# Optimization experiments

Hardware: AMD Instinct MI355X
Metric: run time of the kernel (lower is better)

The kernel has to match this reference:

```python
import jax, jax.numpy as jnp
import numpy as np
import math

B, H, W, C = 8, 32, 32, 512
NUM_HEAD_CHANNELS = 64
NUM_HEADS = C // NUM_HEAD_CHANNELS  # 8
HEAD_DIM = C // NUM_HEADS            # 64
NUM_GROUPS = max(1, C // 16)         # 32
EPS = 1e-6  # flax GroupNorm default epsilon


def setup_inputs() -> dict:
    key = jax.random.key(0)
    ks = jax.random.split(key, 7)
    s = lambda fan: 1.0 / math.sqrt(fan)
    return {
        "x": jax.random.normal(ks[0], (B, H, W, C), jnp.float32),
        "gn_scale": jnp.ones((C,), jnp.float32),
        "gn_bias": jnp.zeros((C,), jnp.float32),
        "w_qkv": jax.random.normal(ks[1], (C, 3 * C), jnp.float32) * s(C),
        "b_qkv": jnp.zeros((3 * C,), jnp.float32),
        "w_out": jax.random.normal(ks[2], (C, C), jnp.float32) * s(C),
        "b_out": jnp.zeros((C,), jnp.float32),
    }


def _group_norm(x, scale, bias):
    # x: (B,H,W,C); normalize per (batch, group) over spatial + in-group channels
    b, h, w, c = x.shape
    xg = x.reshape(b, h * w, NUM_GROUPS, c // NUM_GROUPS)
    mu = jnp.mean(xg, axis=(1, 3), keepdims=True)
    var = jnp.var(xg, axis=(1, 3), keepdims=True)
    xn = (xg - mu) * jax.lax.rsqrt(var + EPS)
    return xn.reshape(b, h, w, c) * scale + bias


def reference(x, gn_scale, gn_bias, w_qkv, b_qkv, w_out, b_out):
    b, h, w, c = x.shape
    seq = h * w
    x_flat = x.reshape(b, seq, c)
    x_norm = _group_norm(x, gn_scale, gn_bias).reshape(b, seq, c)
    qkv = x_norm @ w_qkv + b_qkv                      # (b, seq, 3c)
    q, k, v = jnp.split(qkv, 3, axis=-1)
    scale = 1.0 / math.sqrt(HEAD_DIM)

    def to_heads(t):
        return t.reshape(b, seq, NUM_HEADS, HEAD_DIM).transpose(0, 2, 1, 3)

    q, k, v = to_heads(q), to_heads(k), to_heads(v)
    # NOTE: scale applied to both q and k, matching the original module
    weight = jnp.einsum('bhld,bhsd->bhls', q * scale, k * scale)
    weight = jax.nn.softmax(weight, axis=-1)
    out = jnp.einsum('bhls,bhsd->bhld', weight, v)
    out = out.transpose(0, 2, 1, 3).reshape(b, seq, c)
    out = out @ w_out + b_out
    return (x_flat + out).reshape(b, h, w, c)
```

## Files before the change

kernel.cpp:

```cpp
#include <hip/hip_runtime.h>
#include <hip/hip_bf16.h>

#define SEQ   1024
#define CH    512
#define NHEAD 8
#define HDIM  64
#define BATCH 8

using short8  = __attribute__((ext_vector_type(8))) short;
using short4v = __attribute__((ext_vector_type(4))) short;
using floatx4 = __attribute__((ext_vector_type(4))) float;

__device__ inline unsigned short f2bf(float f) {
  __hip_bfloat16 h = __float2bfloat16(f);
  return __builtin_bit_cast(unsigned short, h);
}

__device__ inline void load_lds16(const void* g, void* l) {
  __builtin_amdgcn_global_load_lds(
      (const __attribute__((address_space(1))) unsigned int*)g,
      (__attribute__((address_space(3))) unsigned int*)l, 16, 0, 0);
}

__global__ __launch_bounds__(256) void prep_kernel(
    const float* __restrict__ wqkv, const float* __restrict__ wout,
    const float* __restrict__ x, const float* __restrict__ gsc,
    const float* __restrict__ gbs,
    unsigned short* __restrict__ wqkvt, unsigned short* __restrict__ woutt,
    unsigned short* __restrict__ xn) {
  __shared__ float SH[32 * 33 + 8];
  const int blk = blockIdx.x, tid = threadIdx.x;

  if (blk >= 256) {
    const float* src; unsigned short* dst; int C, bx, by;
    if (blk < 1024) { int t = blk - 256; src = wqkv; dst = wqkvt; C = 1536; bx = t % 48; by = t / 48; }
    else { int t = blk - 1024; src = wout; dst = woutt; C = 512; bx = t & 15; by = t >> 4; }
    float (*T)[33] = (float(*)[33])SH;
    int tx = tid & 31, ty = tid >> 5;
    for (int j = 0; j < 4; ++j)
      T[ty + j * 8][tx] = src[(size_t)(by * 32 + ty + j * 8) * C + bx * 32 + tx];
    __syncthreads();
    for (int j = 0; j < 4; ++j)
      dst[(size_t)(bx * 32 + ty + j * 8) * 512 + by * 32 + tx] = f2bf(T[tx][ty + j * 8]);
    return;
  }

  int bg = blk;
  int b = bg >> 5, g = bg & 31;
  const size_t base = (size_t)b * SEQ * CH + g * 16;

  float4 v[16];
  float s = 0.f, sq = 0.f;
  for (int i = 0; i < 16; ++i) {
    int c = i * 256 + tid;
    int r = c >> 2, c4 = (c & 3) * 4;
    v[i] = *(const float4*)(x + base + (size_t)r * CH + c4);
    s  += v[i].x + v[i].y + v[i].z + v[i].w;
    sq += v[i].x * v[i].x + v[i].y * v[i].y + v[i].z * v[i].z + v[i].w * v[i].w;
  }
  for (int off = 1; off < 64; off <<= 1) {
    s  += __shfl_xor(s, off);
    sq += __shfl_xor(sq, off);
  }
  float* ls = SH + 1056;
  float* lq = SH + 1060;
  int wid = tid >> 6, lane = tid & 63;
  if (lane == 0) { ls[wid] = s; lq[wid] = sq; }
  __syncthreads();
  float ts = ls[0] + ls[1] + ls[2] + ls[3];
  float tq = lq[0] + lq[1] + lq[2] + lq[3];
  const float inv_n = 1.0f / 16384.0f;
  float mean = ts * inv_n;
  float var  = tq * inv_n - mean * mean;
  float rstd = rsqrtf(var + 1e-6f);

  int c4 = (tid & 3) * 4;
  float4 sc = *(const float4*)(gsc + g * 16 + c4);
  float4 bs = *(const float4*)(gbs + g * 16 + c4);
  for (int i = 0; i < 16; ++i) {
    int c = i * 256 + tid;
    int r = c >> 2;
    ushort4 o;
    o.x = f2bf((v[i].x - mean) * rstd * sc.x + bs.x);
    o.y = f2bf((v[i].y - mean) * rstd * sc.y + bs.y);
    o.z = f2bf((v[i].z - mean) * rstd * sc.z + bs.z);
    o.w = f2bf((v[i].w - mean) * rstd * sc.w + bs.w);
    *(ushort4*)(xn + (size_t)(b * SEQ + r) * CH + g * 16 + c4) = o;
  }
}

template <int EPI, int MTILE>
__global__ __launch_bounds__(256) void gemm_bt_kernel(
    const unsigned short* __restrict__ A, const unsigned short* __restrict__ Bt,
    int K, int N,
    const float* __restrict__ bias, const float* __restrict__ resid,
    float* __restrict__ outf,
    unsigned short* __restrict__ qb, unsigned short* __restrict__ kb,
    unsigned short* __restrict__ vtb) {
  constexpr int SMSZ = (MTILE == 128) ? 17408 : 16896;
  constexpr int NI   = (MTILE == 128) ? 4 : 2;
  __shared__ alignas(16) unsigned short SM[SMSZ];
  unsigned short* LA = SM;
  unsigned short* LB = SM + MTILE * 64;

  const int tid = threadIdx.x;
  const int wid = tid >> 6, lane = tid & 63;
  const int quad = lane >> 4, m16 = lane & 15;
  const int sw = m16 & 7;
  const int wm = (MTILE == 128) ? (wid & 1) * 64 : 0;
  const int wn = (MTILE == 128) ? (wid >> 1) * 64 : wid * 32;
  const int m0 = blockIdx.y * MTILE, n0 = blockIdx.x * 128;

  floatx4 acc[4][NI];
  for (int i = 0; i < 4; ++i)
    for (int j = 0; j < NI; ++j) acc[i][j] = 0.f;

  for (int k0 = 0; k0 < K; k0 += 64) {
    for (int i = 0; i < MTILE / 32; ++i) {
      int c = i * 256 + tid;
      int r = c >> 3, kc = c & 7;
      load_lds16(A + (size_t)(m0 + r) * K + k0 + ((kc ^ (r & 7)) << 3), &LA[c << 3]);
    }
    for (int i = 0; i < 4; ++i) {
      int c = i * 256 + tid;
      int r = c >> 3, kc = c & 7;
      load_lds16(Bt + (size_t)(n0 + r) * K + k0 + ((kc ^ (r & 7)) << 3), &LB[c << 3]);
    }
    __syncthreads();
    for (int kq = 0; kq < 2; ++kq) {
      int csw = (((kq << 2) + quad) ^ sw) << 3;
      short8 af[4], bf[NI];
      for (int mi = 0; mi < 4; ++mi)
        af[mi] = *(const short8*)&LA[(wm + mi * 16 + m16) * 64 + csw];
      for (int ni = 0; ni < NI; ++ni)
        bf[ni] = *(const short8*)&LB[(wn + ni * 16 + m16) * 64 + csw];
      for (int mi = 0; mi < 4; ++mi)
        for (int ni = 0; ni < NI; ++ni)
          acc[mi][ni] = __builtin_amdgcn_mfma_f32_16x16x32_bf16(af[mi], bf[ni], acc[mi][ni], 0, 0, 0);
    }
    __syncthreads();
  }

  const int b = m0 >> 10;
  if (EPI == 0) {
    const int part = blockIdx.x >> 2;
    if (part < 2) {
      const float qscale = (part == 0) ? 0.0225421381f : 1.0f;
      unsigned short* dst = (part == 0) ? qb : kb;
      for (int mi = 0; mi < 4; ++mi)
        for (int ni = 0; ni < 4; ++ni) {
          int ln = wn + ni * 16 + m16;
          float bb = bias[n0 + ln];
          for (int reg = 0; reg < 4; ++reg)
            SM[(wm + mi * 16 + quad * 4 + reg) * 136 + ln] =
                f2bf((acc[mi][ni][reg] + bb) * qscale);
        }
      __syncthreads();
      const int colb = n0 & 511;
      for (int j = 0; j < 8; ++j) {
        int c = j * 256 + tid;
        int m = c >> 4, n8 = (c & 15) * 8;
        int h = (colb + n8) >> 6, d = n8 & 63;
        int sp = (m0 & 1023) + m;
        int4 v = *(const int4*)&SM[m * 136 + n8];
        *(int4*)(dst + (((size_t)(b * NHEAD + h)) * SEQ + sp) * HDIM + d) = v;
      }
    } else {
      for (int mi = 0; mi < 4; ++mi)
        for (int ni = 0; ni < 4; ++ni) {
          int ln = wn + ni * 16 + m16;
          float bb = bias[n0 + ln];
          int mblk = (wm >> 4) + mi;
          int sbase = 32 * (mblk >> 1) + 8 * quad + 4 * (mblk & 1);
          for (int reg = 0; reg < 4; ++reg)
            SM[ln * 136 + sbase + reg] = f2bf(acc[mi][ni][reg] + bb);
        }
      __syncthreads();
      int hbase = (n0 - 1024) >> 6;
      for (int j = 0; j < 8; ++j) {
        int c = j * 256 + tid;
        int ld = c >> 4, sp8 = (c & 15) * 8;
        int h = hbase + (ld >> 6), d = ld & 63;
        int4 v = *(const int4*)&SM[ld * 136 + sp8];
        *(int4*)(vtb + ((size_t)(b * NHEAD + h) * HDIM + d) * SEQ + (m0 & 1023) + sp8) = v;
      }
    }
  } else {
    float* SMf = (float*)SM;
    for (int mi = 0; mi < 4; ++mi)
      for (int ni = 0; ni < NI; ++ni) {
        int ln = wn + ni * 16 + m16;
        float bb = bias[n0 + ln];
        for (int reg = 0; reg < 4; ++reg)
          SMf[(mi * 16 + quad * 4 + reg) * 132 + ln] = acc[mi][ni][reg] + bb;
      }
    __syncthreads();
    for (int j = 0; j < 8; ++j) {
      int c = j * 256 + tid;
      int m = c >> 5, n4 = (c & 31) * 4;
      size_t idx = (size_t)(m0 + m) * N + n0 + n4;
      float4 v = *(const float4*)&SMf[m * 132 + n4];
      float4 rr = *(const float4*)&resid[idx];
      v.x += rr.x; v.y += rr.y; v.z += rr.z; v.w += rr.w;
      *(float4*)&outf[idx] = v;
    }
  }
}

__global__ __launch_bounds__(512) void attn_kernel(
    const unsigned short* __restrict__ qb, const unsigned short* __restrict__ kb,
    const unsigned short* __restrict__ vtb, unsigned short* __restrict__ ao) {
  const int qt = blockIdx.x, head = blockIdx.y;
  const int b = head >> 3, h = head & 7;
  const int tid = threadIdx.x;
  const int wid = tid >> 6, lane = tid & 63;
  const int quad = lane >> 4, m16 = lane & 15;
  const int sw = m16 & 7;

  __shared__ alignas(16) unsigned short sK[8192];
  __shared__ alignas(16) unsigned short sV[8192];

  const unsigned short* kbase = kb  + (size_t)head * SEQ * HDIM;
  const unsigned short* vbase = vtb + (size_t)head * HDIM * SEQ;

  const size_t qrow = (size_t)head * SEQ + qt * 128 + wid * 16 + m16;
  short8 aq0 = *(const short8*)(qb + qrow * HDIM + quad * 8);
  short8 aq1 = *(const short8*)(qb + qrow * HDIM + 32 + quad * 8);

  float lacc = 0.f;
  floatx4 o[4];
  for (int df = 0; df < 4; ++df) o[df] = 0.f;

  for (int kt = 0; kt < 8; ++kt) {
    for (int i = 0; i < 2; ++i) {
      int c = i * 512 + tid;
      int r = c >> 3, kc = c & 7;
      load_lds16(kbase + (kt * 128 + r) * HDIM + ((kc ^ (r & 7)) << 3), &sK[c << 3]);
    }
    for (int i = 0; i < 2; ++i) {
      int c = i * 512 + tid;
      int d = c >> 4, kc = c & 15;
      load_lds16(vbase + d * SEQ + kt * 128 + ((kc ^ (d & 7)) << 3), &sV[c << 3]);
    }
    __syncthreads();

    short8 pf32[4];
    for (int sf = 0; sf < 8; ++sf) {
      const int rb = (sf * 16 + m16) * 64;
      short8 k0 = *(const short8*)&sK[rb + ((quad ^ sw) << 3)];
      short8 k1 = *(const short8*)&sK[rb + (((4 + quad) ^ sw) << 3)];
      floatx4 s = 0.f;
      s = __builtin_amdgcn_mfma_f32_16x16x32_bf16(k0, aq0, s, 0, 0, 0);
      s = __builtin_amdgcn_mfma_f32_16x16x32_bf16(k1, aq1, s, 0, 0, 0);
      const int u = sf >> 1, t4 = (sf & 1) * 4;
      for (int r = 0; r < 4; ++r) {
        float p = exp2f(s[r]);
        lacc += p;
        pf32[u][t4 + r] = (short)f2bf(p);
      }
    }

    for (int u = 0; u < 4; ++u) {
      const int chunk = ((u * 4 + quad) ^ sw) << 3;
      for (int df = 0; df < 4; ++df) {
        short8 bv = *(const short8*)&sV[(df * 16 + m16) * 128 + chunk];
        o[df] = __builtin_amdgcn_mfma_f32_16x16x32_bf16(pf32[u], bv, o[df], 0, 0, 0);
      }
    }
    __syncthreads();
  }

  lacc += __shfl_xor(lacc, 16);
  lacc += __shfl_xor(lacc, 32);
  lacc = 1.0f / lacc;
  float l0 = __shfl(lacc, quad * 4 + 0);
  float l1 = __shfl(lacc, quad * 4 + 1);
  float l2 = __shfl(lacc, quad * 4 + 2);
  float l3 = __shfl(lacc, quad * 4 + 3);
  int qg = qt * 128 + wid * 16 + quad * 4;
  for (int df = 0; df < 4; ++df) {
    int col = h * HDIM + df * 16 + m16;
    size_t base = (size_t)(b * SEQ + qg) * CH + col;
    ao[base + 0 * CH] = f2bf(o[df][0] * l0);
    ao[base + 1 * CH] = f2bf(o[df][1] * l1);
    ao[base + 2 * CH] = f2bf(o[df][2] * l2);
    ao[base + 3 * CH] = f2bf(o[df][3] * l3);
  }
}

extern "C" void kernel_launch(void* const* d_in, const int* in_sizes, int n_in,
                              void* d_out, int out_size, void* d_ws, size_t ws_size,
                              hipStream_t stream) {
  const float* x    = (const float*)d_in[0];
  const float* gsc  = (const float*)d_in[1];
  const float* gbs  = (const float*)d_in[2];
  const float* wqkv = (const float*)d_in[3];
  const float* bqkv = (const float*)d_in[4];
  const float* wout = (const float*)d_in[5];
  const float* bout = (const float*)d_in[6];
  float* out = (float*)d_out;

  char* ws = (char*)d_ws;
  unsigned short* xn    = (unsigned short*)(ws);
  unsigned short* wqkvt = (unsigned short*)(ws + 8388608);
  unsigned short* woutt = (unsigned short*)(ws + 9961472);
  unsigned short* qb    = (unsigned short*)(ws + 10485760);
  unsigned short* kb    = (unsigned short*)(ws + 18874368);
  unsigned short* vtb   = (unsigned short*)(ws + 27262976);
  unsigned short* ao    = (unsigned short*)(ws + 35651584);

  prep_kernel<<<1280, 256, 0, stream>>>(wqkv, wout, x, gsc, gbs, wqkvt, woutt, xn);
  gemm_bt_kernel<0, 128><<<dim3(12, 64), 256, 0, stream>>>(
      xn, wqkvt, 512, 1536, bqkv, nullptr, nullptr, qb, kb, vtb);
  attn_kernel<<<dim3(8, 64), 512, 0, stream>>>(qb, kb, vtb, ao);
  gemm_bt_kernel<1, 64><<<dim3(4, 128), 256, 0, stream>>>(
      ao, woutt, 512, 512, bout, x, out, nullptr, nullptr, nullptr);
}
```

Measured before the change: 154.2 us.

## Split group-norm into chunked stats and apply kernels; reorder grid dimensions

Group-norm now runs in two kernels. The first computes partial sums over 128-row chunks across 2048 blocks instead of 256, and the second applies the normalization per chunk using the combined stats. The goal is to expose far more parallelism than one block per (batch, group) over 1024 rows. In exchange, x is read twice and an extra launch is added. The grid axes of the QKV GEMM, attention and output GEMM are also swapped, which changes block scheduling order and may affect L2 reuse of weights and K/V.

```diff
diff --git a/kernel.cpp b/kernel.cpp
--- a/kernel.cpp
+++ b/kernel.cpp
@@ -22,19 +22,18 @@
       (__attribute__((address_space(3))) unsigned int*)l, 16, 0, 0);
 }
 
-__global__ __launch_bounds__(256) void prep_kernel(
+__global__ __launch_bounds__(256) void prep_stats_kernel(
     const float* __restrict__ wqkv, const float* __restrict__ wout,
-    const float* __restrict__ x, const float* __restrict__ gsc,
-    const float* __restrict__ gbs,
+    const float* __restrict__ x,
     unsigned short* __restrict__ wqkvt, unsigned short* __restrict__ woutt,
-    unsigned short* __restrict__ xn) {
+    float2* __restrict__ stats) {
   __shared__ float SH[32 * 33 + 8];
   const int blk = blockIdx.x, tid = threadIdx.x;
 
-  if (blk >= 256) {
+  if (blk >= 2048) {
     const float* src; unsigned short* dst; int C, bx, by;
-    if (blk < 1024) { int t = blk - 256; src = wqkv; dst = wqkvt; C = 1536; bx = t % 48; by = t / 48; }
-    else { int t = blk - 1024; src = wout; dst = woutt; C = 512; bx = t & 15; by = t >> 4; }
+    if (blk < 2816) { int t = blk - 2048; src = wqkv; dst = wqkvt; C = 1536; bx = t % 48; by = t / 48; }
+    else { int t = blk - 2816; src = wout; dst = woutt; C = 512; bx = t & 15; by = t >> 4; }
     float (*T)[33] = (float(*)[33])SH;
     int tx = tid & 31, ty = tid >> 5;
     for (int j = 0; j < 4; ++j)
@@ -45,18 +44,17 @@
     return;
   }
 
-  int bg = blk;
-  int b = bg >> 5, g = bg & 31;
-  const size_t base = (size_t)b * SEQ * CH + g * 16;
-
-  float4 v[16];
+  const int bg = blk >> 3, chunk = blk & 7;
+  const int b = bg >> 5, g = bg & 31;
+  const size_t base = (size_t)b * SEQ * CH + (size_t)chunk * 128 * CH + g * 16;
+
   float s = 0.f, sq = 0.f;
-  for (int i = 0; i < 16; ++i) {
+  for (int i = 0; i < 2; ++i) {
     int c = i * 256 + tid;
     int r = c >> 2, c4 = (c & 3) * 4;
-    v[i] = *(const float4*)(x + base + (size_t)r * CH + c4);
-    s  += v[i].x + v[i].y + v[i].z + v[i].w;
-    sq += v[i].x * v[i].x + v[i].y * v[i].y + v[i].z * v[i].z + v[i].w * v[i].w;
+    float4 v = *(const float4*)(x + base + (size_t)r * CH + c4);
+    s  += v.x + v.y + v.z + v.w;
+    sq += v.x * v.x + v.y * v.y + v.z * v.z + v.w * v.w;
   }
   for (int off = 1; off < 64; off <<= 1) {
     s  += __shfl_xor(s, off);
@@ -67,25 +65,47 @@
   int wid = tid >> 6, lane = tid & 63;
   if (lane == 0) { ls[wid] = s; lq[wid] = sq; }
   __syncthreads();
-  float ts = ls[0] + ls[1] + ls[2] + ls[3];
-  float tq = lq[0] + lq[1] + lq[2] + lq[3];
+  if (tid == 0) {
+    float2 p;
+    p.x = ls[0] + ls[1] + ls[2] + ls[3];
+    p.y = lq[0] + lq[1] + lq[2] + lq[3];
+    stats[(bg << 3) + chunk] = p;
+  }
+}
+
+__global__ __launch_bounds__(256) void prep_apply_kernel(
+    const float* __restrict__ x, const float* __restrict__ gsc,
+    const float* __restrict__ gbs, const float2* __restrict__ stats,
+    unsigned short* __restrict__ xn) {
+  const int blk = blockIdx.x, tid = threadIdx.x;
+  const int bg = blk >> 3, chunk = blk & 7;
+  const int b = bg >> 5, g = bg & 31;
+
+  float ts = 0.f, tq = 0.f;
+  for (int i = 0; i < 8; ++i) {
+    float2 p = stats[(bg << 3) + i];
+    ts += p.x; tq += p.y;
+  }
   const float inv_n = 1.0f / 16384.0f;
   float mean = ts * inv_n;
   float var  = tq * inv_n - mean * mean;
   float rstd = rsqrtf(var + 1e-6f);
 
+  const size_t base = (size_t)b * SEQ * CH + (size_t)chunk * 128 * CH + g * 16;
+  const size_t obase = (size_t)(b * SEQ + chunk * 128) * CH + g * 16;
   int c4 = (tid & 3) * 4;
   float4 sc = *(const float4*)(gsc + g * 16 + c4);
   float4 bs = *(const float4*)(gbs + g * 16 + c4);
-  for (int i = 0; i < 16; ++i) {
+  for (int i = 0; i < 2; ++i) {
     int c = i * 256 + tid;
     int r = c >> 2;
+    float4 v = *(const float4*)(x + base + (size_t)r * CH + c4);
     ushort4 o;
-    o.x = f2bf((v[i].x - mean) * rstd * sc.x + bs.x);
-    o.y = f2bf((v[i].y - mean) * rstd * sc.y + bs.y);
-    o.z = f2bf((v[i].z - mean) * rstd * sc.z + bs.z);
-    o.w = f2bf((v[i].w - mean) * rstd * sc.w + bs.w);
-    *(ushort4*)(xn + (size_t)(b * SEQ + r) * CH + g * 16 + c4) = o;
+    o.x = f2bf((v.x - mean) * rstd * sc.x + bs.x);
+    o.y = f2bf((v.y - mean) * rstd * sc.y + bs.y);
+    o.z = f2bf((v.z - mean) * rstd * sc.z + bs.z);
+    o.w = f2bf((v.w - mean) * rstd * sc.w + bs.w);
+    *(ushort4*)(xn + obase + (size_t)r * CH + c4) = o;
   }
 }
 
@@ -109,7 +129,7 @@
   const int sw = m16 & 7;
   const int wm = (MTILE == 128) ? (wid & 1) * 64 : 0;
   const int wn = (MTILE == 128) ? (wid >> 1) * 64 : wid * 32;
-  const int m0 = blockIdx.y * MTILE, n0 = blockIdx.x * 128;
+  const int m0 = blockIdx.x * MTILE, n0 = blockIdx.y * 128;
 
   floatx4 acc[4][NI];
   for (int i = 0; i < 4; ++i)
@@ -143,7 +163,7 @@
 
   const int b = m0 >> 10;
   if (EPI == 0) {
-    const int part = blockIdx.x >> 2;
+    const int part = n0 >> 9;
     if (part < 2) {
       const float qscale = (part == 0) ? 0.0225421381f : 1.0f;
       unsigned short* dst = (part == 0) ? qb : kb;
@@ -210,7 +230,7 @@
 __global__ __launch_bounds__(512) void attn_kernel(
     const unsigned short* __restrict__ qb, const unsigned short* __restrict__ kb,
     const unsigned short* __restrict__ vtb, unsigned short* __restrict__ ao) {
-  const int qt = blockIdx.x, head = blockIdx.y;
+  const int head = blockIdx.x, qt = blockIdx.y;
   const int b = head >> 3, h = head & 7;
   const int tid = threadIdx.x;
   const int wid = tid >> 6, lane = tid & 63;
@@ -308,11 +328,13 @@
   unsigned short* kb    = (unsigned short*)(ws + 18874368);
   unsigned short* vtb   = (unsigned short*)(ws + 27262976);
   unsigned short* ao    = (unsigned short*)(ws + 35651584);
-
-  prep_kernel<<<1280, 256, 0, stream>>>(wqkv, wout, x, gsc, gbs, wqkvt, woutt, xn);
-  gemm_bt_kernel<0, 128><<<dim3(12, 64), 256, 0, stream>>>(
+  float2*         stats = (float2*)(ws + 44040192);
+
+  prep_stats_kernel<<<3072, 256, 0, stream>>>(wqkv, wout, x, wqkvt, woutt, stats);
+  prep_apply_kernel<<<2048, 256, 0, stream>>>(x, gsc, gbs, stats, xn);
+  gemm_bt_kernel<0, 128><<<dim3(64, 12), 256, 0, stream>>>(
       xn, wqkvt, 512, 1536, bqkv, nullptr, nullptr, qb, kb, vtb);
-  attn_kernel<<<dim3(8, 64), 512, 0, stream>>>(qb, kb, vtb, ao);
-  gemm_bt_kernel<1, 64><<<dim3(4, 128), 256, 0, stream>>>(
+  attn_kernel<<<dim3(64, 8), 512, 0, stream>>>(qb, kb, vtb, ao);
+  gemm_bt_kernel<1, 64><<<dim3(128, 4), 256, 0, stream>>>(
       ao, woutt, 512, 512, bout, x, out, nullptr, nullptr, nullptr);
 }
```

Result: faster. 150.2 us (-2.6%).
